# Optimization experiments

Hardware: AMD Instinct MI355X
Metric: run time of the kernel (lower is better)

Reference implementation:

```python
import jax, jax.numpy as jnp
import numpy as np

B, S, D, H = 2, 2048, 1024, 16
DK = D // H  # 64


def setup_inputs() -> dict:
    key = jax.random.key(0)
    ks = jax.random.split(key, 5)
    std = 0.02
    return {
        "x": jax.random.normal(ks[0], (B, S, D), dtype=jnp.float32),
        "Wq": jax.random.normal(ks[1], (D, D), dtype=jnp.float32) * std,
        "bq": jnp.zeros((D,), jnp.float32),
        "Wk": jax.random.normal(ks[2], (D, D), dtype=jnp.float32) * std,
        "bk": jnp.zeros((D,), jnp.float32),
        "Wv": jax.random.normal(ks[3], (D, D), dtype=jnp.float32) * std,
        "bv": jnp.zeros((D,), jnp.float32),
        "Wo": jax.random.normal(ks[4], (D, D), dtype=jnp.float32) * std,
        "bo": jnp.zeros((D,), jnp.float32),
    }


def reference(x, Wq, bq, Wk, bk, Wv, bv, Wo, bo):
    b, s, d = x.shape
    # QKV projections (torch Linear: x @ W.T + b)
    q = x @ Wq.T + bq
    k = x @ Wk.T + bk
    v = x @ Wv.T + bv
    # [b, s, d] -> [b, h, s, d_k]
    q = q.reshape(b, s, H, DK).transpose(0, 2, 1, 3)
    k = k.reshape(b, s, H, DK).transpose(0, 2, 1, 3)
    v = v.reshape(b, s, H, DK).transpose(0, 2, 1, 3)
    # scaled dot-product scores [b, h, s, s]
    scores = jnp.einsum('bhqd,bhkd->bhqk', q, k) / np.float32(np.sqrt(DK))
    # causal mask (mask=True path in original forward)
    causal = jnp.tril(jnp.ones((s, s), dtype=bool))
    scores = jnp.where(causal, scores, jnp.float32(-1e9))
    attn = jax.nn.softmax(scores, axis=-1)
    # dropout is identity in eval / p=0
    out = jnp.einsum('bhqk,bhkd->bhqd', attn, v)
    out = out.transpose(0, 2, 1, 3).reshape(b, s, d)
    return out @ Wo.T + bo
```

## Files before the change

### kernel.cpp

```cpp
#include <hip/hip_runtime.h>
#include <stdint.h>
#include <math.h>

#define B_ 2
#define S_ 2048
#define D_ 1024
#define H_ 16
#define DK_ 64
#define M_ (B_*S_)

typedef unsigned short u16;
typedef unsigned int u32;
typedef __attribute__((ext_vector_type(8))) __bf16 bf16x8;
typedef __attribute__((ext_vector_type(4))) float f32x4;

#define AS1 __attribute__((address_space(1)))
#define AS3 __attribute__((address_space(3)))

__device__ __forceinline__ u16 f2bf(float f) {
  u32 u = __float_as_uint(f);
  return (u16)((u + 0x7fffu + ((u >> 16) & 1u)) >> 16);
}
__device__ __forceinline__ u16 f2bfr(float f) {
  return (u16)((__float_as_uint(f) + 0x8000u) >> 16);
}

__device__ __forceinline__ void gload_lds16(const void* g, void* lds) {
  __builtin_amdgcn_global_load_lds((const AS1 u32*)g,
                                   (AS3 u32*)(u32)(uintptr_t)lds, 16, 0, 0);
}

__global__ __launch_bounds__(256) void f2bf_kernel(const float* __restrict__ in,
                                                   u16* __restrict__ out, int n4) {
  int i = blockIdx.x * 256 + threadIdx.x;
  if (i >= n4) return;
  float4 v = ((const float4*)in)[i];
  u32 lo = (u32)f2bf(v.x) | ((u32)f2bf(v.y) << 16);
  u32 hi = (u32)f2bf(v.z) | ((u32)f2bf(v.w) << 16);
  ((uint2*)out)[i] = make_uint2(lo, hi);
}

__global__ __launch_bounds__(256) void f2bf4_kernel(
    const float* __restrict__ W0, const float* __restrict__ W1,
    const float* __restrict__ W2, const float* __restrict__ W3,
    u16* __restrict__ o0, u16* __restrict__ o1, u16* __restrict__ o2, u16* __restrict__ o3,
    int n4) {
  const float* src; u16* dst;
  switch (blockIdx.y) {
    case 0: src = W0; dst = o0; break;
    case 1: src = W1; dst = o1; break;
    case 2: src = W2; dst = o2; break;
    default: src = W3; dst = o3; break;
  }
  int i = blockIdx.x * 256 + threadIdx.x;
  if (i >= n4) return;
  float4 v = ((const float4*)src)[i];
  u32 lo = (u32)f2bf(v.x) | ((u32)f2bf(v.y) << 16);
  u32 hi = (u32)f2bf(v.z) | ((u32)f2bf(v.w) << 16);
  ((uint2*)dst)[i] = make_uint2(lo, hi);
}

template <bool OUT_F32, bool QKV>
__global__ __launch_bounds__(256) void gemm_bt(
    const u16* __restrict__ A,
    const u16* __restrict__ W0, const u16* __restrict__ W1, const u16* __restrict__ W2,
    const float* __restrict__ b0, const float* __restrict__ b1, const float* __restrict__ b2,
    void* __restrict__ C0, void* __restrict__ C1, void* __restrict__ C2,
    int M, int N, int K) {
  const u16* W = W0; const float* bias = b0; void* Cv = C0;
  float osc = 1.0f;
  if (QKV) {
    if (blockIdx.z == 0)      { osc = 0.18033688f; }
    else if (blockIdx.z == 1) { W = W1; bias = b1; Cv = C1; }
    else                      { W = W2; bias = b2; Cv = C2; }
  }
  __shared__ u16 As[128*32];
  __shared__ u16 Bs[128*32];
  const int tid = threadIdx.x;
  const int wave = tid >> 6, lane = tid & 63;
  const int lo = lane & 15, hi = lane >> 4;
  const int wr = wave >> 1, wc = wave & 1;
  const int mbase = blockIdx.y * 128, nbase = blockIdx.x * 128;

  f32x4 acc[4][4] = {};

  for (int k0 = 0; k0 < K; k0 += 32) {
#pragma unroll
    for (int i = 0; i < 2; ++i) {
      int row = i*64 + (tid >> 2);
      int col = (tid & 3) * 8;
      gload_lds16(&A[(size_t)(mbase + row)*K + k0 + col], &As[row*32 + col]);
      gload_lds16(&W[(size_t)(nbase + row)*K + k0 + col], &Bs[row*32 + col]);
    }
    __syncthreads();
    bf16x8 af[4], bfr[4];
#pragma unroll
    for (int m = 0; m < 4; ++m)
      af[m] = *(const bf16x8*)&As[(wr*64 + m*16 + lo)*32 + hi*8];
#pragma unroll
    for (int n = 0; n < 4; ++n)
      bfr[n] = *(const bf16x8*)&Bs[(wc*64 + n*16 + lo)*32 + hi*8];
#pragma unroll
    for (int m = 0; m < 4; ++m)
#pragma unroll
      for (int n = 0; n < 4; ++n)
        acc[m][n] = __builtin_amdgcn_mfma_f32_16x16x32_bf16(af[m], bfr[n], acc[m][n], 0, 0, 0);
    __syncthreads();
  }

#pragma unroll
  for (int n = 0; n < 4; ++n) {
    int col = nbase + wc*64 + n*16 + lo;
    float bv = bias[col];
#pragma unroll
    for (int m = 0; m < 4; ++m) {
#pragma unroll
      for (int j = 0; j < 4; ++j) {
        int row = mbase + wr*64 + m*16 + hi*4 + j;
        float v = (acc[m][n][j] + bv) * osc;
        if constexpr (OUT_F32) ((float*)Cv)[(size_t)row*N + col] = v;
        else                   ((u16*)Cv)[(size_t)row*N + col] = f2bf(v);
      }
    }
  }
}

__global__ __launch_bounds__(256) void gemm_bt64(
    const u16* __restrict__ A, const u16* __restrict__ W,
    const float* __restrict__ bias, float* __restrict__ C,
    int M, int N, int K) {
  __shared__ u16 As[64*32];
  __shared__ u16 Bs[128*32];
  const int tid = threadIdx.x;
  const int wave = tid >> 6, lane = tid & 63;
  const int lo = lane & 15, hi = lane >> 4;
  const int mbase = blockIdx.y * 64, nbase = blockIdx.x * 128;

  f32x4 acc[4][2] = {};

  for (int k0 = 0; k0 < K; k0 += 32) {
    {
      int row = tid >> 2;
      int col = (tid & 3) * 8;
      gload_lds16(&A[(size_t)(mbase + row)*K + k0 + col], &As[row*32 + col]);
#pragma unroll
      for (int i = 0; i < 2; ++i)
        gload_lds16(&W[(size_t)(nbase + i*64 + row)*K + k0 + col], &Bs[(i*64 + row)*32 + col]);
    }
    __syncthreads();
    bf16x8 af[4], bfr[2];
#pragma unroll
    for (int m = 0; m < 4; ++m)
      af[m] = *(const bf16x8*)&As[(m*16 + lo)*32 + hi*8];
#pragma unroll
    for (int n = 0; n < 2; ++n)
      bfr[n] = *(const bf16x8*)&Bs[(wave*32 + n*16 + lo)*32 + hi*8];
#pragma unroll
    for (int m = 0; m < 4; ++m)
#pragma unroll
      for (int n = 0; n < 2; ++n)
        acc[m][n] = __builtin_amdgcn_mfma_f32_16x16x32_bf16(af[m], bfr[n], acc[m][n], 0, 0, 0);
    __syncthreads();
  }

#pragma unroll
  for (int n = 0; n < 2; ++n) {
    int col = nbase + wave*32 + n*16 + lo;
    float bv = bias[col];
#pragma unroll
    for (int m = 0; m < 4; ++m)
#pragma unroll
      for (int j = 0; j < 4; ++j) {
        int row = mbase + m*16 + hi*4 + j;
        C[(size_t)row*N + col] = acc[m][n][j] + bv;
      }
  }
}

__global__ __launch_bounds__(256) void transpose_v(const u16* __restrict__ V,
                                                   u16* __restrict__ Vt) {
  const int st = blockIdx.x, bh = blockIdx.y;
  const int b = bh >> 4, h = bh & 15;
  __shared__ u16 tile[64][72];
  const int tid = threadIdx.x;
#pragma unroll
  for (int c = 0; c < 2; ++c) {
    int s = c*32 + (tid >> 3);
    int d0 = (tid & 7) * 8;
    *(uint4*)&tile[s][d0] =
        *(const uint4*)&V[((size_t)(b*S_ + st*64 + s))*D_ + h*DK_ + d0];
  }
  __syncthreads();
#pragma unroll
  for (int c = 0; c < 2; ++c) {
    int d = c*32 + (tid >> 3);
    int s0 = (tid & 7) * 8;
    uint4 ov;
    u16* tp = (u16*)&ov;
#pragma unroll
    for (int jj = 0; jj < 8; ++jj) tp[jj] = tile[s0 + jj][d];
    *(uint4*)&Vt[((size_t)(bh*DK_ + d))*S_ + st*64 + s0] = ov;
  }
}

__global__ __launch_bounds__(256) void attn_kernel(
    const u16* __restrict__ Q, const u16* __restrict__ K, const u16* __restrict__ Vt,
    u16* __restrict__ AO) {
  const int blk = blockIdx.x;
  const int xcd = blk & 7, slot = blk >> 3;
  const int bh = xcd + 8*(slot & 3);
  const int qt = 31 - (slot >> 2);
  const int b = bh >> 4, h = bh & 15;
  const int tid = threadIdx.x, w = tid >> 6, lane = tid & 63;
  const int lo = lane & 15, hi = lane >> 4;

  __shared__ u16 Kl[2][64*64];
  __shared__ u16 Vl[2][64*64];
  __shared__ u16 Pl[4][16*72];

  const int r8 = lane >> 3;
  const int rloc = w*8 + r8;
  const int xorcol = ((lane & 7) ^ r8) * 8;
  const size_t kbase = (size_t)b*S_*D_ + (size_t)h*DK_;
  const size_t vbase = (size_t)bh*DK_*S_;
  const size_t koff0 = kbase + (size_t)rloc*D_ + xorcol;
  const size_t koff1 = kbase + (size_t)(32 + rloc)*D_ + xorcol;
  const size_t voff0 = vbase + (size_t)rloc*S_ + xorcol;
  const size_t voff1 = vbase + (size_t)(32 + rloc)*S_ + xorcol;
  const int ldsoff = rloc*64 + (lane & 7)*8;

  const int qrow = qt*64 + w*16 + lo;
  bf16x8 qf[2];
#pragma unroll
  for (int kk = 0; kk < 2; ++kk)
    qf[kk] = *(const bf16x8*)&Q[(size_t)(b*S_ + qrow)*D_ + h*DK_ + kk*32 + hi*8];

  f32x4 o[4] = {};
  float mr = -INFINITY, lr = 0.f;

  gload_lds16(&K[koff0], &Kl[0][ldsoff]);
  gload_lds16(&K[koff1], &Kl[0][2048 + ldsoff]);
  gload_lds16(&Vt[voff0], &Vl[0][ldsoff]);
  gload_lds16(&Vt[voff1], &Vl[0][2048 + ldsoff]);

  for (int kt = 0; kt <= qt; ++kt) {
    const int cur = kt & 1;
    __syncthreads();
    if (kt < qt) {
      const size_t kadd = (size_t)(kt + 1)*64*D_;
      const int vadd = (kt + 1)*64;
      gload_lds16(&K[koff0 + kadd], &Kl[cur ^ 1][ldsoff]);
      gload_lds16(&K[koff1 + kadd], &Kl[cur ^ 1][2048 + ldsoff]);
      gload_lds16(&Vt[voff0 + vadd], &Vl[cur ^ 1][ldsoff]);
      gload_lds16(&Vt[voff1 + vadd], &Vl[cur ^ 1][2048 + ldsoff]);
    }

    f32x4 s[4] = {};
#pragma unroll
    for (int kk = 0; kk < 2; ++kk) {
#pragma unroll
      for (int n = 0; n < 4; ++n) {
        int row = n*16 + lo;
        bf16x8 kf = *(const bf16x8*)&Kl[cur][row*64 + (((kk*4 + hi) ^ (row & 7)) * 8)];
        s[n] = __builtin_amdgcn_mfma_f32_16x16x32_bf16(kf, qf[kk], s[n], 0, 0, 0);
      }
    }

    if (kt == qt) {
      const int ql = w*16 + lo;
#pragma unroll
      for (int n = 0; n < 4; ++n)
#pragma unroll
        for (int j = 0; j < 4; ++j)
          if (n*16 + hi*4 + j > ql) s[n][j] = -INFINITY;
    }

    float pm = -INFINITY;
#pragma unroll
    for (int n = 0; n < 4; ++n)
#pragma unroll
      for (int j = 0; j < 4; ++j) pm = fmaxf(pm, s[n][j]);

    if (!__all(pm <= mr + 11.0f)) {
      pm = fmaxf(pm, __shfl_xor(pm, 16));
      pm = fmaxf(pm, __shfl_xor(pm, 32));
      float mn = fmaxf(mr, pm);
      float corr = __builtin_amdgcn_exp2f(mr - mn);
      mr = mn;
      lr *= corr;
      float cj[4];
#pragma unroll
      for (int j = 0; j < 4; ++j) cj[j] = __shfl(corr, hi*4 + j);
#pragma unroll
      for (int n = 0; n < 4; ++n)
#pragma unroll
        for (int j = 0; j < 4; ++j) o[n][j] *= cj[j];
    }

#pragma unroll
    for (int n = 0; n < 4; ++n) {
      float p0 = __builtin_amdgcn_exp2f(s[n][0] - mr);
      float p1 = __builtin_amdgcn_exp2f(s[n][1] - mr);
      float p2 = __builtin_amdgcn_exp2f(s[n][2] - mr);
      float p3 = __builtin_amdgcn_exp2f(s[n][3] - mr);
      lr += (p0 + p1) + (p2 + p3);
      u32 d01 = (u32)f2bfr(p0) | ((u32)f2bfr(p1) << 16);
      u32 d23 = (u32)f2bfr(p2) | ((u32)f2bfr(p3) << 16);
      *(uint2*)&Pl[w][lo*72 + n*16 + hi*4] = make_uint2(d01, d23);
    }

#pragma unroll
    for (int kk = 0; kk < 2; ++kk) {
      bf16x8 pf = *(const bf16x8*)&Pl[w][lo*72 + kk*32 + hi*8];
#pragma unroll
      for (int n = 0; n < 4; ++n) {
        int row = n*16 + lo;
        bf16x8 vf = *(const bf16x8*)&Vl[cur][row*64 + (((kk*4 + hi) ^ (row & 7)) * 8)];
        o[n] = __builtin_amdgcn_mfma_f32_16x16x32_bf16(pf, vf, o[n], 0, 0, 0);
      }
    }
  }

  lr += __shfl_xor(lr, 16);
  lr += __shfl_xor(lr, 32);
  float rinv[4];
#pragma unroll
  for (int j = 0; j < 4; ++j) rinv[j] = __builtin_amdgcn_rcpf(__shfl(lr, hi*4 + j));
#pragma unroll
  for (int n = 0; n < 4; ++n)
#pragma unroll
    for (int j = 0; j < 4; ++j) {
      int rowg = qt*64 + w*16 + hi*4 + j;
      AO[(size_t)(b*S_ + rowg)*D_ + h*DK_ + n*16 + lo] = f2bf(o[n][j] * rinv[j]);
    }
}

extern "C" void kernel_launch(void* const* d_in, const int* in_sizes, int n_in,
                              void* d_out, int out_size, void* d_ws, size_t ws_size,
                              hipStream_t stream) {
  const float* x  = (const float*)d_in[0];
  const float* Wq = (const float*)d_in[1];
  const float* bq = (const float*)d_in[2];
  const float* Wk = (const float*)d_in[3];
  const float* bk = (const float*)d_in[4];
  const float* Wv = (const float*)d_in[5];
  const float* bv = (const float*)d_in[6];
  const float* Wo = (const float*)d_in[7];
  const float* bo = (const float*)d_in[8];

  char* ws = (char*)d_ws;
  const size_t MB = 1048576;
  u16* xb  = (u16*)(ws + 0);
  u16* Wqb = (u16*)(ws + 8*MB);
  u16* Wkb = (u16*)(ws + 10*MB);
  u16* Wvb = (u16*)(ws + 12*MB);
  u16* Wob = (u16*)(ws + 14*MB);
  u16* Qb  = (u16*)(ws + 16*MB);
  u16* Kb  = (u16*)(ws + 24*MB);
  u16* Vb  = (u16*)(ws + 32*MB);
  u16* Vtb = (u16*)(ws + 0);
  u16* AOb = (u16*)(ws + 32*MB);

  f2bf_kernel<<<4096, 256, 0, stream>>>(x, xb, (M_*D_)/4);
  f2bf4_kernel<<<dim3(1024, 4), 256, 0, stream>>>(Wq, Wk, Wv, Wo,
                                                  Wqb, Wkb, Wvb, Wob, (D_*D_)/4);

  gemm_bt<false, true><<<dim3(8, 32, 3), 256, 0, stream>>>(
      xb, Wqb, Wkb, Wvb, bq, bk, bv, Qb, Kb, Vb, M_, D_, D_);

  transpose_v<<<dim3(32, 32), 256, 0, stream>>>(Vb, Vtb);

  attn_kernel<<<1024, 256, 0, stream>>>(Qb, Kb, Vtb, AOb);

  gemm_bt64<<<dim3(8, 64), 256, 0, stream>>>(AOb, Wob, bo, (float*)d_out, M_, D_, D_);
}
```

Before: 118.1 us.

## Replace QKV GEMM with 256x256 double-buffered eight-phase pipelined kernel

Swaps the 128x128, K=32 single-buffered QKV projection GEMM for a 512-thread kernel that computes 256x256 tiles with K=64 steps. It double-buffers LDS with XOR-swizzled layout and splits each K step into eight phases that interleave async global-to-LDS loads with MFMA work, gated by explicit vmcnt waits and setprio. Blocks are remapped so tiles sharing A rows land on the same XCD. This aims to hide memory latency and raise data reuse per load. In exchange it runs only 192 workgroups at one block per CU, so on a 256-CU part some CUs sit idle, and the hand-counted wait sequence is fragile.

```diff
diff --git a/kernel.cpp b/kernel.cpp
--- a/kernel.cpp
+++ b/kernel.cpp
@@ -8,6 +8,7 @@
 #define H_ 16
 #define DK_ 64
 #define M_ (B_*S_)
+#define NT_ 16
 
 typedef unsigned short u16;
 typedef unsigned int u32;
@@ -29,6 +30,13 @@
   __builtin_amdgcn_global_load_lds((const AS1 u32*)g,
                                    (AS3 u32*)(u32)(uintptr_t)lds, 16, 0, 0);
 }
+
+__device__ __forceinline__ f32x4 mfma16(bf16x8 a, bf16x8 b, f32x4 c) {
+  return __builtin_amdgcn_mfma_f32_16x16x32_bf16(a, b, c, 0, 0, 0);
+}
+
+#define VMCNT_(n) asm volatile("s_waitcnt vmcnt(" #n ")" ::: "memory")
+#define VMCNT(n) VMCNT_(n)
 
 __global__ __launch_bounds__(256) void f2bf_kernel(const float* __restrict__ in,
                                                    u16* __restrict__ out, int n4) {
@@ -60,69 +68,119 @@
   ((uint2*)dst)[i] = make_uint2(lo, hi);
 }
 
-template <bool OUT_F32, bool QKV>
-__global__ __launch_bounds__(256) void gemm_bt(
+__global__ __launch_bounds__(512, 1) void gemm_qkv_8ph(
     const u16* __restrict__ A,
     const u16* __restrict__ W0, const u16* __restrict__ W1, const u16* __restrict__ W2,
     const float* __restrict__ b0, const float* __restrict__ b1, const float* __restrict__ b2,
-    void* __restrict__ C0, void* __restrict__ C1, void* __restrict__ C2,
-    int M, int N, int K) {
-  const u16* W = W0; const float* bias = b0; void* Cv = C0;
-  float osc = 1.0f;
-  if (QKV) {
-    if (blockIdx.z == 0)      { osc = 0.18033688f; }
-    else if (blockIdx.z == 1) { W = W1; bias = b1; Cv = C1; }
-    else                      { W = W2; bias = b2; Cv = C2; }
-  }
-  __shared__ u16 As[128*32];
-  __shared__ u16 Bs[128*32];
+    u16* __restrict__ C0, u16* __restrict__ C1, u16* __restrict__ C2) {
+  const int id = blockIdx.x;
+  const int xcd = id & 7, k = id >> 3;
+  const int my = xcd*2 + (k & 1);
+  const int rest = k >> 1;
+  const int z = rest >> 2, nx = rest & 3;
+
+  const u16* W = (z == 0) ? W0 : (z == 1) ? W1 : W2;
+  const float* bias = (z == 0) ? b0 : (z == 1) ? b1 : b2;
+  u16* C = (z == 0) ? C0 : (z == 1) ? C1 : C2;
+  const float osc = (z == 0) ? 0.18033688f : 1.0f;
+  const int mbase = my*256, nbase = nx*256;
+
+  __shared__ u16 LA[2][256*64];
+  __shared__ u16 LB[2][256*64];
+
   const int tid = threadIdx.x;
-  const int wave = tid >> 6, lane = tid & 63;
+  const int w = tid >> 6, lane = tid & 63;
   const int lo = lane & 15, hi = lane >> 4;
-  const int wr = wave >> 1, wc = wave & 1;
-  const int mbase = blockIdx.y * 128, nbase = blockIdx.x * 128;
-
-  f32x4 acc[4][4] = {};
-
-  for (int k0 = 0; k0 < K; k0 += 32) {
-#pragma unroll
-    for (int i = 0; i < 2; ++i) {
-      int row = i*64 + (tid >> 2);
-      int col = (tid & 3) * 8;
-      gload_lds16(&A[(size_t)(mbase + row)*K + k0 + col], &As[row*32 + col]);
-      gload_lds16(&W[(size_t)(nbase + row)*K + k0 + col], &Bs[row*32 + col]);
-    }
-    __syncthreads();
-    bf16x8 af[4], bfr[4];
-#pragma unroll
-    for (int m = 0; m < 4; ++m)
-      af[m] = *(const bf16x8*)&As[(wr*64 + m*16 + lo)*32 + hi*8];
-#pragma unroll
-    for (int n = 0; n < 4; ++n)
-      bfr[n] = *(const bf16x8*)&Bs[(wc*64 + n*16 + lo)*32 + hi*8];
-#pragma unroll
-    for (int m = 0; m < 4; ++m)
-#pragma unroll
-      for (int n = 0; n < 4; ++n)
-        acc[m][n] = __builtin_amdgcn_mfma_f32_16x16x32_bf16(af[m], bfr[n], acc[m][n], 0, 0, 0);
-    __syncthreads();
+  const int wr = w >> 2, wc = w & 3;
+
+  const int sr = tid >> 3;
+  const int sc = tid & 7;
+  const int sx = (sc ^ (sr & 7)) * 8;
+
+#define STAGE_A(buf, t, h) do {                                                   \
+    int gr_ = sr + (h)*64;                                                        \
+    size_t g_ = (size_t)(mbase + gr_)*D_ + (size_t)(t)*64 + sx;                   \
+    gload_lds16(&A[g_],            &LA[buf][gr_*64 + sc*8]);                      \
+    gload_lds16(&A[g_ + 128*D_],   &LA[buf][(gr_ + 128)*64 + sc*8]);              \
+  } while (0)
+
+#define STAGE_B(buf, t, h) do {                                                   \
+    int gr_ = (sr & 31) + (h)*32 + (sr >> 5)*64;                                  \
+    size_t g_ = (size_t)(nbase + gr_)*D_ + (size_t)(t)*64 + sx;                   \
+    gload_lds16(&W[g_],            &LB[buf][gr_*64 + sc*8]);                      \
+    gload_lds16(&W[g_ + 128*D_],   &LB[buf][(gr_ + 128)*64 + sc*8]);              \
+  } while (0)
+
+  f32x4 acc[8][4] = {};
+
+#define PHASE(buf, mq, nq, STAGE_STMT, WAIT_STMT) do {                            \
+    bf16x8 af_[4][2], bv_[2][2];                                                  \
+    _Pragma("unroll")                                                             \
+    for (int m_ = 0; m_ < 4; ++m_) {                                              \
+      int R_ = wr*128 + (mq)*64 + m_*16 + lo;                                     \
+      int rx_ = R_ & 7, base_ = R_*64;                                            \
+      af_[m_][0] = *(const bf16x8*)&LA[buf][base_ + ((hi ^ rx_) * 8)];            \
+      af_[m_][1] = *(const bf16x8*)&LA[buf][base_ + (((4 + hi) ^ rx_) * 8)];      \
+    }                                                                             \
+    _Pragma("unroll")                                                             \
+    for (int n_ = 0; n_ < 2; ++n_) {                                              \
+      int R_ = wc*64 + (nq)*32 + n_*16 + lo;                                      \
+      int rx_ = R_ & 7, base_ = R_*64;                                            \
+      bv_[n_][0] = *(const bf16x8*)&LB[buf][base_ + ((hi ^ rx_) * 8)];            \
+      bv_[n_][1] = *(const bf16x8*)&LB[buf][base_ + (((4 + hi) ^ rx_) * 8)];      \
+    }                                                                             \
+    STAGE_STMT;                                                                   \
+    WAIT_STMT;                                                                    \
+    __builtin_amdgcn_s_barrier();                                                 \
+    __builtin_amdgcn_s_setprio(1);                                                \
+    _Pragma("unroll")                                                             \
+    for (int m_ = 0; m_ < 4; ++m_)                                                \
+      _Pragma("unroll")                                                           \
+      for (int n_ = 0; n_ < 2; ++n_) {                                            \
+        acc[(mq)*4 + m_][(nq)*2 + n_] =                                           \
+            mfma16(af_[m_][0], bv_[n_][0], acc[(mq)*4 + m_][(nq)*2 + n_]);        \
+        acc[(mq)*4 + m_][(nq)*2 + n_] =                                           \
+            mfma16(af_[m_][1], bv_[n_][1], acc[(mq)*4 + m_][(nq)*2 + n_]);        \
+      }                                                                           \
+    __builtin_amdgcn_s_setprio(0);                                                \
+    __builtin_amdgcn_s_barrier();                                                 \
+  } while (0)
+
+  STAGE_A(0, 0, 0); STAGE_B(0, 0, 0);
+  STAGE_A(0, 0, 1); STAGE_B(0, 0, 1);
+  STAGE_A(1, 1, 0); STAGE_B(1, 1, 0);
+  VMCNT(8);
+  __builtin_amdgcn_s_barrier();
+
+  for (int j = 0; j < NT_/2; ++j) {
+    const int t1 = 2*j + 1;
+    const int tp0 = (2*j + 2 < NT_) ? 2*j + 2 : NT_ - 1;
+    const int tp1 = (2*j + 3 < NT_) ? 2*j + 3 : NT_ - 1;
+    PHASE(0, 0, 0, STAGE_A(1, t1, 1),  VMCNT(6));
+    PHASE(0, 0, 1, STAGE_B(1, t1, 1),  (void)0);
+    PHASE(0, 1, 0, STAGE_A(0, tp0, 0), (void)0);
+    PHASE(0, 1, 1, STAGE_B(0, tp0, 0), VMCNT(8));
+    PHASE(1, 0, 0, STAGE_A(0, tp0, 1), VMCNT(6));
+    PHASE(1, 0, 1, STAGE_B(0, tp0, 1), (void)0);
+    PHASE(1, 1, 0, STAGE_A(1, tp1, 0), (void)0);
+    PHASE(1, 1, 1, STAGE_B(1, tp1, 0), VMCNT(8));
   }
 
 #pragma unroll
   for (int n = 0; n < 4; ++n) {
     int col = nbase + wc*64 + n*16 + lo;
-    float bv = bias[col];
-#pragma unroll
-    for (int m = 0; m < 4; ++m) {
-#pragma unroll
-      for (int j = 0; j < 4; ++j) {
-        int row = mbase + wr*64 + m*16 + hi*4 + j;
-        float v = (acc[m][n][j] + bv) * osc;
-        if constexpr (OUT_F32) ((float*)Cv)[(size_t)row*N + col] = v;
-        else                   ((u16*)Cv)[(size_t)row*N + col] = f2bf(v);
+    float bv2 = bias[col];
+#pragma unroll
+    for (int m = 0; m < 8; ++m)
+#pragma unroll
+      for (int jj = 0; jj < 4; ++jj) {
+        int row = mbase + wr*128 + m*16 + hi*4 + jj;
+        C[(size_t)row*D_ + col] = f2bf((acc[m][n][jj] + bv2) * osc);
       }
-    }
-  }
+  }
+#undef PHASE
+#undef STAGE_A
+#undef STAGE_B
 }
 
 __global__ __launch_bounds__(256) void gemm_bt64(
@@ -365,8 +423,7 @@
   f2bf4_kernel<<<dim3(1024, 4), 256, 0, stream>>>(Wq, Wk, Wv, Wo,
                                                   Wqb, Wkb, Wvb, Wob, (D_*D_)/4);
 
-  gemm_bt<false, true><<<dim3(8, 32, 3), 256, 0, stream>>>(
-      xb, Wqb, Wkb, Wvb, bq, bk, bv, Qb, Kb, Vb, M_, D_, D_);
+  gemm_qkv_8ph<<<192, 512, 0, stream>>>(xb, Wqb, Wkb, Wvb, bq, bk, bv, Qb, Kb, Vb);
 
   transpose_v<<<dim3(32, 32), 256, 0, stream>>>(Vb, Vtb);
 
```

Result: faster. 114.6 us (-3.0%).
